# Kernel tuning notes

Hardware: AMD Instinct MI355X
Metric: run time of the kernel (lower is better)

The kernel has to match this reference:

```python
import jax, jax.numpy as jnp
import numpy as np
from jax import lax

PHI_WIDTH = 1.0  # default width of the Phi play-operator

def _phi(x):
    # Phi(x) = max(0, x) + min(0, x + width)
    return jnp.maximum(0.0, x) + jnp.minimum(0.0, x + PHI_WIDTH)

def setup_inputs() -> dict:
    key = jax.random.key(0)
    T = 16_777_216  # number of recurrence steps; input has T+1 entries
    inputs = jax.random.normal(key, (T + 1,), dtype=jnp.float32)
    kernel = jnp.float32(1.0)  # scalar trainable weight (self.weight = 1.0)
    return {"inputs": inputs, "kernel": kernel}

def reference(inputs, kernel):
    # p0 is the initial state; remaining entries are the driving signal
    p0 = inputs[0]
    x = inputs[1:] * kernel  # [T]

    def step(y_prev, xt):
        y = _phi(xt - y_prev) + y_prev
        return y, y

    _, ys = lax.scan(step, p0, x)  # ys: [T]
    return jnp.concatenate([p0[None], ys])  # [T+1], matches tf.convert_to_tensor(outputs)
```

## Files before the change

kernel.cpp:

```cpp
#include <hip/hip_runtime.h>
#include <math.h>


#define TPB 256
#define EPT 16
#define EPB (TPB * EPT)
#define XP 17
#define HCH 256

struct Pair { float a, b; };

__device__ __forceinline__ float med3f(float x, float lo, float hi) {
    return __builtin_amdgcn_fmed3f(x, lo, hi);
}
__device__ __forceinline__ Pair compose(Pair l, Pair r) {
    Pair o; o.a = med3f(l.a, r.a, r.b); o.b = med3f(l.b, r.a, r.b); return o;
}
__device__ __forceinline__ Pair ident() {
    Pair p; p.a = -INFINITY; p.b = INFINITY; return p;
}

__global__ __launch_bounds__(TPB)
void k_scan(const float* __restrict__ in, const float* __restrict__ kptr,
            float* __restrict__ out, int n) {
    const int tid  = threadIdx.x, lane = tid & 63, wid = tid >> 6;
    const int vid  = blockIdx.x;
    const int tile0 = vid * EPB;
    const int base  = tile0 + tid * EPT;
    const float k   = kptr[0];
    const bool blockFull = (tile0 + EPB <= n);

    __shared__ Pair  wS[TPB / 64];
    __shared__ Pair  wC[TPB / 64];
    __shared__ float xpose[TPB * XP];

    float ta[EPT], tb[EPT];
    {
        float a = -INFINITY, b = INFINITY;
        if (blockFull) {
            #pragma unroll
            for (int v = 0; v < EPT / 4; ++v) {
                float4 f = reinterpret_cast<const float4*>(in + base)[v];
                float xv[4] = {f.x, f.y, f.z, f.w};
                #pragma unroll
                for (int jj = 0; jj < 4; ++jj) {
                    float lo = xv[jj] * k, hi = lo + 1.0f;
                    if (v == 0 && jj == 0 && base == 0) { lo = xv[0]; hi = xv[0]; }
                    a = med3f(a, lo, hi);
                    b = med3f(b, lo, hi);
                    ta[4*v+jj] = a; tb[4*v+jj] = b;
                }
            }
        } else {
            #pragma unroll
            for (int j = 0; j < EPT; ++j) {
                if (base + j < n) {
                    float x = in[base + j];
                    float lo = x * k, hi = lo + 1.0f;
                    if (j == 0 && base == 0) { lo = x; hi = x; }
                    a = med3f(a, lo, hi);
                    b = med3f(b, lo, hi);
                }
                ta[j] = a; tb[j] = b;
            }
        }
    }

    Pair w; w.a = ta[EPT - 1]; w.b = tb[EPT - 1];
    #pragma unroll
    for (int off = 1; off < 64; off <<= 1) {
        Pair u; u.a = __shfl_up(w.a, off); u.b = __shfl_up(w.b, off);
        if (lane >= off) w = compose(u, w);
    }
    if (lane == 63) wS[wid] = w;
    __syncthreads();
    Pair wpre = ident();
    #pragma unroll
    for (int i = 0; i < TPB / 64; ++i) if (i < wid) wpre = compose(wpre, wS[i]);
    Pair up; up.a = __shfl_up(w.a, 1); up.b = __shfl_up(w.b, 1);
    Pair ex = (lane == 0) ? wpre : compose(wpre, up);

    Pair S = ident();
    int chunkEnd = tile0;
    while (chunkEnd > 0) {
        int chunkStart = chunkEnd - HCH; if (chunkStart < 0) chunkStart = 0;
        const int count = chunkEnd - chunkStart;
        const int e = chunkStart + tid;
        Pair wnd = ident();
        if (tid < count) {
            float x = in[e];
            float lo = x * k, hi = lo + 1.0f;
            if (e == 0) { lo = x; hi = x; }
            wnd.a = lo; wnd.b = hi;
        }
        #pragma unroll
        for (int off = 1; off < 64; off <<= 1) {
            Pair u; u.a = __shfl_down(wnd.a, off); u.b = __shfl_down(wnd.b, off);
            Pair c = compose(wnd, u);
            if (lane + off < 64) wnd = c;
        }
        if (lane == 0) wC[wid] = wnd;
        __syncthreads();
        Pair cagg = wC[0];
        #pragma unroll
        for (int i = 1; i < TPB / 64; ++i) cagg = compose(cagg, wC[i]);
        __syncthreads();
        S = compose(cagg, S);
        if (S.a == S.b) break;
        chunkEnd = chunkStart;
    }
    const float ysrc = med3f(0.0f, S.a, S.b);

    const float ytin = med3f(ysrc, ex.a, ex.b);
    if (blockFull) {
        #pragma unroll
        for (int j = 0; j < EPT; ++j)
            xpose[tid * XP + j] = med3f(ytin, ta[j], tb[j]);
        __syncthreads();
        #pragma unroll
        for (int c4 = 0; c4 < EPT / 4; ++c4) {
            const int q4    = c4 * (TPB * 4) + 4 * tid;
            const int owner = q4 >> 4;
            const int slot  = q4 & 15;
            float4 f;
            f.x = xpose[owner * XP + slot + 0];
            f.y = xpose[owner * XP + slot + 1];
            f.z = xpose[owner * XP + slot + 2];
            f.w = xpose[owner * XP + slot + 3];
            reinterpret_cast<float4*>(out + tile0)[c4 * TPB + tid] = f;
        }
    } else {
        #pragma unroll
        for (int j = 0; j < EPT; ++j)
            if (base + j < n) out[base + j] = med3f(ytin, ta[j], tb[j]);
    }
}

extern "C" void kernel_launch(void* const* d_in, const int* in_sizes, int n_in,
                              void* d_out, int out_size, void* d_ws, size_t ws_size,
                              hipStream_t stream) {
    const float* in   = (const float*)d_in[0];
    const float* kptr = (const float*)d_in[1];
    float* out = (float*)d_out;
    const int n  = in_sizes[0];
    const int nb = (n + EPB - 1) / EPB;

    k_scan<<<nb, TPB, 0, stream>>>(in, kptr, out, n);
}
```

Before: 26.41 us.

## Shrink per-thread tile to one float4 and drop LDS transpose for stores

Reduces elements per thread from 16 to 4, so each thread loads and stores a single contiguous float4. That makes the shared-memory transpose for coalesced writes unnecessary, which removes one barrier and the LDS staging buffer. The look-back chunk loop also drops its partial-chunk bounds check, since tile starts are now multiples of the chunk size. The cost is four times as many blocks, each running its own backward look-back over previous chunks, which adds redundant global reads and per-block overhead.

```diff
diff --git a/kernel.cpp b/kernel.cpp
--- a/kernel.cpp
+++ b/kernel.cpp
@@ -3,10 +3,10 @@
 
 
 #define TPB 256
-#define EPT 16
+#define EPT 4
 #define EPB (TPB * EPT)
-#define XP 17
-#define HCH 256
+#define NW  (TPB / 64)
+#define HCH TPB
 
 struct Pair { float a, b; };
 
@@ -30,26 +30,22 @@
     const float k   = kptr[0];
     const bool blockFull = (tile0 + EPB <= n);
 
-    __shared__ Pair  wS[TPB / 64];
-    __shared__ Pair  wC[TPB / 64];
-    __shared__ float xpose[TPB * XP];
+    __shared__ Pair wS[NW];
+    __shared__ Pair wC[NW];
 
     float ta[EPT], tb[EPT];
     {
         float a = -INFINITY, b = INFINITY;
         if (blockFull) {
+            float4 f = *reinterpret_cast<const float4*>(in + base);
+            float xv[4] = {f.x, f.y, f.z, f.w};
             #pragma unroll
-            for (int v = 0; v < EPT / 4; ++v) {
-                float4 f = reinterpret_cast<const float4*>(in + base)[v];
-                float xv[4] = {f.x, f.y, f.z, f.w};
-                #pragma unroll
-                for (int jj = 0; jj < 4; ++jj) {
-                    float lo = xv[jj] * k, hi = lo + 1.0f;
-                    if (v == 0 && jj == 0 && base == 0) { lo = xv[0]; hi = xv[0]; }
-                    a = med3f(a, lo, hi);
-                    b = med3f(b, lo, hi);
-                    ta[4*v+jj] = a; tb[4*v+jj] = b;
-                }
+            for (int j = 0; j < 4; ++j) {
+                float lo = xv[j] * k, hi = lo + 1.0f;
+                if (j == 0 && base == 0) { lo = xv[0]; hi = xv[0]; }
+                a = med3f(a, lo, hi);
+                b = med3f(b, lo, hi);
+                ta[j] = a; tb[j] = b;
             }
         } else {
             #pragma unroll
@@ -76,19 +72,18 @@
     __syncthreads();
     Pair wpre = ident();
     #pragma unroll
-    for (int i = 0; i < TPB / 64; ++i) if (i < wid) wpre = compose(wpre, wS[i]);
+    for (int i = 0; i < NW; ++i) if (i < wid) wpre = compose(wpre, wS[i]);
     Pair up; up.a = __shfl_up(w.a, 1); up.b = __shfl_up(w.b, 1);
     Pair ex = (lane == 0) ? wpre : compose(wpre, up);
 
     Pair S = ident();
     int chunkEnd = tile0;
     while (chunkEnd > 0) {
-        int chunkStart = chunkEnd - HCH; if (chunkStart < 0) chunkStart = 0;
-        const int count = chunkEnd - chunkStart;
+        const int chunkStart = chunkEnd - HCH;
         const int e = chunkStart + tid;
-        Pair wnd = ident();
-        if (tid < count) {
-            float x = in[e];
+        Pair wnd;
+        {
+            float x  = in[e];
             float lo = x * k, hi = lo + 1.0f;
             if (e == 0) { lo = x; hi = x; }
             wnd.a = lo; wnd.b = hi;
@@ -103,7 +98,7 @@
         __syncthreads();
         Pair cagg = wC[0];
         #pragma unroll
-        for (int i = 1; i < TPB / 64; ++i) cagg = compose(cagg, wC[i]);
+        for (int i = 1; i < NW; ++i) cagg = compose(cagg, wC[i]);
         __syncthreads();
         S = compose(cagg, S);
         if (S.a == S.b) break;
@@ -113,22 +108,12 @@
 
     const float ytin = med3f(ysrc, ex.a, ex.b);
     if (blockFull) {
-        #pragma unroll
-        for (int j = 0; j < EPT; ++j)
-            xpose[tid * XP + j] = med3f(ytin, ta[j], tb[j]);
-        __syncthreads();
-        #pragma unroll
-        for (int c4 = 0; c4 < EPT / 4; ++c4) {
-            const int q4    = c4 * (TPB * 4) + 4 * tid;
-            const int owner = q4 >> 4;
-            const int slot  = q4 & 15;
-            float4 f;
-            f.x = xpose[owner * XP + slot + 0];
-            f.y = xpose[owner * XP + slot + 1];
-            f.z = xpose[owner * XP + slot + 2];
-            f.w = xpose[owner * XP + slot + 3];
-            reinterpret_cast<float4*>(out + tile0)[c4 * TPB + tid] = f;
-        }
+        float4 o;
+        o.x = med3f(ytin, ta[0], tb[0]);
+        o.y = med3f(ytin, ta[1], tb[1]);
+        o.z = med3f(ytin, ta[2], tb[2]);
+        o.w = med3f(ytin, ta[3], tb[3]);
+        *reinterpret_cast<float4*>(out + base) = o;
     } else {
         #pragma unroll
         for (int j = 0; j < EPT; ++j)
```

Result: slower. 32.07 us (+21.5%).
